# Optimization experiments

Measured on AMD Instinct MI355X. Metric: run time of the kernel, lower is better.

Reference implementation:

```python
import jax, jax.numpy as jnp
import numpy as np

B, S, H, NH = 1, 2048, 2048, 16
HD = H // NH
EPS = 1e-5
NEG = jnp.finfo(jnp.float32).min


def _alibi_slopes(n_heads):
    # standard Bloom alibi slopes (n_heads power of 2)
    start = 2.0 ** (-(2.0 ** -(np.log2(n_heads) - 3)))
    return start * (start ** np.arange(n_heads))


def setup_inputs() -> dict:
    key = jax.random.key(0)
    ks = jax.random.split(key, 10)
    s = 0.02
    hidden_states = jax.random.normal(ks[0], (B, S, H), jnp.float32)
    # causal mask: True = masked (future positions)
    causal = ~jnp.tril(jnp.ones((S, S), dtype=bool))
    attention_mask = causal[None, None, :, :]  # [1,1,S,S]
    # alibi bias [B*NH, 1, S]
    slopes = jnp.asarray(_alibi_slopes(NH), jnp.float32)  # [NH]
    pos = jnp.arange(S, dtype=jnp.float32)
    alibi = (slopes[:, None] * pos[None, :])[:, None, :]  # [NH,1,S]
    alibi = jnp.tile(alibi, (B, 1, 1))  # [B*NH,1,S]
    return {
        "hidden_states": hidden_states,
        "attention_mask": attention_mask,
        "alibi": alibi,
        "head_mask": 0,
        "ln1_g": jnp.ones((H,), jnp.float32),
        "ln1_b": jnp.zeros((H,), jnp.float32),
        "qkv_w": jax.random.normal(ks[1], (3 * H, H), jnp.float32) * s,
        "qkv_b": jnp.zeros((3 * H,), jnp.float32),
        "dense_w": jax.random.normal(ks[2], (H, H), jnp.float32) * s,
        "dense_b": jnp.zeros((H,), jnp.float32),
        "ln2_g": jnp.ones((H,), jnp.float32),
        "ln2_b": jnp.zeros((H,), jnp.float32),
        "fc1_w": jax.random.normal(ks[3], (4 * H, H), jnp.float32) * s,
        "fc1_b": jnp.zeros((4 * H,), jnp.float32),
        "fc2_w": jax.random.normal(ks[4], (H, 4 * H), jnp.float32) * s,
        "fc2_b": jnp.zeros((H,), jnp.float32),
    }


def _ln(x, g, b):
    mu = jnp.mean(x, axis=-1, keepdims=True)
    var = jnp.mean(jnp.square(x - mu), axis=-1, keepdims=True)
    return (x - mu) * jax.lax.rsqrt(var + EPS) * g + b


def _gelu(x):
    # Bloom tanh-approx GELU
    return x * 0.5 * (1.0 + jnp.tanh(0.79788456 * x * (1.0 + 0.044715 * x * x)))


def reference(hidden_states, attention_mask, alibi, head_mask,
              ln1_g, ln1_b, qkv_w, qkv_b, dense_w, dense_b,
              ln2_g, ln2_b, fc1_w, fc1_b, fc2_w, fc2_b):
    b, s, h = hidden_states.shape
    x = _ln(hidden_states, ln1_g, ln1_b)
    residual = hidden_states  # apply_residual_connection_post_layernorm=False

    qkv = x @ qkv_w.T + qkv_b                      # [b,s,3H]
    qkv = qkv.reshape(b, s, NH, 3, HD)             # per-head interleaved
    q, k, v = qkv[..., 0, :], qkv[..., 1, :], qkv[..., 2, :]  # [b,s,nh,hd]

    inv = 1.0 / jnp.sqrt(jnp.float32(HD))
    scores = jnp.einsum('bqnd,bknd->bnqk', q, k) * inv  # [b,nh,s,s]
    scores = scores + alibi.reshape(b, NH, 1, s)
    scores = jnp.where(attention_mask, NEG, scores)
    w = jax.nn.softmax(scores, axis=-1)
    # head_mask == 0 -> falsy in original; no head masking applied
    ctx = jnp.einsum('bnqk,bknd->bqnd', w, v).reshape(b, s, h)
    attn_out = ctx @ dense_w.T + dense_b + residual

    y = _ln(attn_out, ln2_g, ln2_b)
    residual2 = attn_out
    hdn = _gelu(y @ fc1_w.T + fc1_b)
    out = hdn @ fc2_w.T + fc2_b + residual2
    return out
```

## Files before the change

### kernel.cpp

```cpp
#include <hip/hip_runtime.h>
#include <hip/hip_bf16.h>

#define SQ 2048
#define HH 2048
#define NHEAD 16
#define HD 128
#define QKVW (NHEAD*3*HD)

typedef __attribute__((ext_vector_type(8))) short bf16x8;
typedef __attribute__((ext_vector_type(4))) float f32x4;
typedef __attribute__((ext_vector_type(16))) float f32x16;

__device__ inline unsigned short f2bf(float f) {
    union { float f; unsigned u; } x; x.f = f;
    unsigned r = x.u + 0x7FFFu + ((x.u >> 16) & 1u);
    return (unsigned short)(r >> 16);
}

__device__ inline unsigned pack_bf2(float a, float b) {
    return (unsigned)f2bf(a) | ((unsigned)f2bf(b) << 16);
}

__device__ inline float gelu_f(float x) {
    float x3 = x * (1.f + 0.044715f * x * x);
    return 0.5f * x * (1.f + tanhf(0.79788456f * x3));
}

__device__ inline void gld16(void* lds, const void* g) {
    __builtin_amdgcn_global_load_lds(
        (__attribute__((address_space(1))) void*)(g),
        (__attribute__((address_space(3))) void*)(lds), 16, 0, 0);
}

__global__ __launch_bounds__(256) void ln_kernel(
    const float* __restrict__ in, const float* __restrict__ g,
    const float* __restrict__ b, unsigned short* __restrict__ out)
{
    int row = blockIdx.x;
    int t = threadIdx.x, lane = t & 63, wid = t >> 6;
    const float4* rp = (const float4*)(in + (size_t)row * HH);
    float4 v0 = rp[t], v1 = rp[t + 256];
    float s  = v0.x + v0.y + v0.z + v0.w + v1.x + v1.y + v1.z + v1.w;
    float ss = v0.x*v0.x + v0.y*v0.y + v0.z*v0.z + v0.w*v0.w
             + v1.x*v1.x + v1.y*v1.y + v1.z*v1.z + v1.w*v1.w;
    #pragma unroll
    for (int o = 32; o; o >>= 1) { s += __shfl_down(s, o); ss += __shfl_down(ss, o); }
    __shared__ float r0[4], r1[4];
    if (lane == 0) { r0[wid] = s; r1[wid] = ss; }
    __syncthreads();
    s  = r0[0] + r0[1] + r0[2] + r0[3];
    ss = r1[0] + r1[1] + r1[2] + r1[3];
    float mu = s * (1.f / HH);
    float var = ss * (1.f / HH) - mu * mu;
    float rs = rsqrtf(var + 1e-5f);
    float4 g0 = ((const float4*)g)[t], g1 = ((const float4*)g)[t + 256];
    float4 b0 = ((const float4*)b)[t], b1 = ((const float4*)b)[t + 256];
    ushort4 o0, o1;
    o0.x = f2bf((v0.x - mu) * rs * g0.x + b0.x);
    o0.y = f2bf((v0.y - mu) * rs * g0.y + b0.y);
    o0.z = f2bf((v0.z - mu) * rs * g0.z + b0.z);
    o0.w = f2bf((v0.w - mu) * rs * g0.w + b0.w);
    o1.x = f2bf((v1.x - mu) * rs * g1.x + b1.x);
    o1.y = f2bf((v1.y - mu) * rs * g1.y + b1.y);
    o1.z = f2bf((v1.z - mu) * rs * g1.z + b1.z);
    o1.w = f2bf((v1.w - mu) * rs * g1.w + b1.w);
    ushort4* op = (ushort4*)(out + (size_t)row * HH);
    op[t] = o0; op[t + 256] = o1;
}

__global__ __launch_bounds__(256) void reduce4_kernel(
    const float* __restrict__ p0, const float* __restrict__ p1,
    const float* __restrict__ p2, const float* __restrict__ p3,
    const float* __restrict__ res, const float* __restrict__ bias,
    float* __restrict__ out, int n4, int nc4m1)
{
    int i = blockIdx.x * blockDim.x + threadIdx.x;
    int st = gridDim.x * blockDim.x;
    for (; i < n4; i += st) {
        float4 a = ((const float4*)p0)[i];
        float4 b = ((const float4*)p1)[i];
        float4 c = ((const float4*)p2)[i];
        float4 d = ((const float4*)p3)[i];
        float4 r = ((const float4*)res)[i];
        float4 bv = ((const float4*)bias)[i & nc4m1];
        float4 o;
        o.x = a.x + b.x + c.x + d.x + r.x + bv.x;
        o.y = a.y + b.y + c.y + d.y + r.y + bv.y;
        o.z = a.z + b.z + c.z + d.z + r.z + bv.z;
        o.w = a.w + b.w + c.w + d.w + r.w + bv.w;
        ((float4*)out)[i] = o;
    }
}


template<int MODE, int GELU_ON>
__global__ __launch_bounds__(512, 4) void gemm256(
    const unsigned short* __restrict__ A, const float* __restrict__ B,
    const float* __restrict__ bias, void* __restrict__ outp,
    unsigned short* __restrict__ vtb, void* __restrict__ outp_hi,
    int N, int lda, int ldb, int kLen, int CH, int CW)
{
    __shared__ __align__(16) unsigned short Asm[2][256][32];
    __shared__ __align__(16) unsigned short Bsm[2][128][40];

    int t = threadIdx.x, lane = t & 63, wid = t >> 6;
    int lo = lane & 15, hi = lane >> 4;
    int wr = wid >> 2, wc = wid & 3;

    int id = (blockIdx.z * gridDim.y + blockIdx.y) * gridDim.x + blockIdx.x;
    int xcd = id & 7, local = id >> 3;
    int cgx = gridDim.x / CW;
    int cr = xcd / cgx, cc = xcd - cr * cgx;
    int lr = local / CW, lc = local - lr * CW;
    int R  = cr * CH + lr;
    int bn = cc * CW + lc;
    int bm = R % gridDim.y;
    int bz = R / gridDim.y;
    int m0 = bm * 256, n0 = bn * 128;
    int kstart = bz * kLen;
    int nt = kLen >> 5;

    int rA0 = wid * 16 + (lane >> 2);
    int sAc = lane & 3;
    int rB = t >> 2, pB = t & 3;

    const unsigned short* Abase = A + (size_t)m0 * lda + kstart;
    int s0 = (rA0 & 3) ^ ((rA0 >> 2) & 3);
    const unsigned short* Asrc0 = Abase + (size_t)rA0 * lda + ((sAc ^ s0) << 3);
    const unsigned short* Asrc1 = Abase + (size_t)(rA0 + 128) * lda + ((sAc ^ s0) << 3);
    const float* Bsrc = B + (size_t)(n0 + rB) * ldb + kstart + pB * 8;

    {
        float4 b0 = *(const float4*)(Bsrc);
        float4 b1 = *(const float4*)(Bsrc + 4);
        gld16(&Asm[0][wid * 16][0], Asrc0);
        gld16(&Asm[0][128 + wid * 16][0], Asrc1);
        int4 w;
        w.x = (int)pack_bf2(b0.x, b0.y); w.y = (int)pack_bf2(b0.z, b0.w);
        w.z = (int)pack_bf2(b1.x, b1.y); w.w = (int)pack_bf2(b1.z, b1.w);
        *(int4*)&Bsm[0][rB][pB * 8] = w;
        __syncthreads();
    }

    f32x4 acc[8][2] = {};
    for (int u = 0; u < nt; u++) {
        int buf = u & 1, nbuf = buf ^ 1;
        int t1 = (u + 1 < nt) ? u + 1 : u;
        float4 b0 = *(const float4*)(Bsrc + t1 * 32);
        float4 b1 = *(const float4*)(Bsrc + t1 * 32 + 4);
        gld16(&Asm[nbuf][wid * 16][0], Asrc0 + t1 * 32);
        gld16(&Asm[nbuf][128 + wid * 16][0], Asrc1 + t1 * 32);
        __builtin_amdgcn_s_setprio(1);
        const unsigned short (*LA)[32] = Asm[buf];
        const unsigned short (*LB)[40] = Bsm[buf];
        bf16x8 bfr0 = *(const bf16x8*)&LB[wc * 32 + lo][hi * 8];
        bf16x8 bfr1 = *(const bf16x8*)&LB[wc * 32 + 16 + lo][hi * 8];
        #pragma unroll
        for (int i = 0; i < 8; i++) {
            int rA = wr * 128 + i * 16 + lo;
            bf16x8 af = *(const bf16x8*)&LA[rA][(hi ^ ((rA & 3) ^ ((rA >> 2) & 3))) << 3];
            acc[i][0] = __builtin_amdgcn_mfma_f32_16x16x32_bf16(bfr0, af, acc[i][0], 0, 0, 0);
            acc[i][1] = __builtin_amdgcn_mfma_f32_16x16x32_bf16(bfr1, af, acc[i][1], 0, 0, 0);
        }
        __builtin_amdgcn_s_setprio(0);
        int4 w;
        w.x = (int)pack_bf2(b0.x, b0.y); w.y = (int)pack_bf2(b0.z, b0.w);
        w.z = (int)pack_bf2(b1.x, b1.y); w.w = (int)pack_bf2(b1.z, b1.w);
        *(int4*)&Bsm[nbuf][rB][pB * 8] = w;
        __syncthreads();
    }

    if (MODE == 0) {
        float* po = ((bz < 2) ? (float*)outp : (float*)outp_hi)
                  + (size_t)(bz & 1) * SQ * (size_t)N;
        #pragma unroll
        for (int i = 0; i < 8; i++) {
            int gr = m0 + wr * 128 + i * 16 + lo;
            #pragma unroll
            for (int c = 0; c < 2; c++) {
                int gc = n0 + wc * 32 + c * 16 + hi * 4;
                *(f32x4*)&po[(size_t)gr * N + gc] = acc[i][c];
            }
        }
    } else if (MODE == 1) {
        unsigned short* op = (unsigned short*)outp;
        #pragma unroll
        for (int i = 0; i < 8; i++) {
            int gr = m0 + wr * 128 + i * 16 + lo;
            #pragma unroll
            for (int c = 0; c < 2; c++) {
                int gc = n0 + wc * 32 + c * 16 + hi * 4;
                float4 bi = *(const float4*)&bias[gc];
                float v0 = acc[i][c][0] + bi.x, v1 = acc[i][c][1] + bi.y;
                float v2 = acc[i][c][2] + bi.z, v3 = acc[i][c][3] + bi.w;
                if (GELU_ON) { v0 = gelu_f(v0); v1 = gelu_f(v1); v2 = gelu_f(v2); v3 = gelu_f(v3); }
                ushort4 o; o.x = f2bf(v0); o.y = f2bf(v1); o.z = f2bf(v2); o.w = f2bf(v3);
                *(ushort4*)&op[(size_t)gr * N + gc] = o;
            }
        }
    } else {
        unsigned short* op = (unsigned short*)outp;
        int head = n0 / 384;
        int cat = (n0 >> 7) % 3;
        #pragma unroll
        for (int i = 0; i < 8; i++) {
            int gr = m0 + wr * 128 + i * 16 + lo;
            #pragma unroll
            for (int c = 0; c < 2; c++) {
                int gc = n0 + wc * 32 + c * 16 + hi * 4;
                float4 bi = *(const float4*)&bias[gc];
                float v0 = acc[i][c][0] + bi.x, v1 = acc[i][c][1] + bi.y;
                float v2 = acc[i][c][2] + bi.z, v3 = acc[i][c][3] + bi.w;
                if (cat == 2) {
                    int d = wc * 32 + c * 16 + hi * 4;
                    unsigned short* vp = vtb + (size_t)(head * HD + d) * SQ + gr;
                    vp[0]      = f2bf(v0);
                    vp[SQ]     = f2bf(v1);
                    vp[2 * SQ] = f2bf(v2);
                    vp[3 * SQ] = f2bf(v3);
                } else {
                    ushort4 o; o.x = f2bf(v0); o.y = f2bf(v1); o.z = f2bf(v2); o.w = f2bf(v3);
                    *(ushort4*)&op[(size_t)gr * N + gc] = o;
                }
            }
        }
    }
}

__global__ __launch_bounds__(128) void attn_kernel(
    const unsigned short* __restrict__ qkvB,
    const unsigned short* __restrict__ vtb,
    unsigned short* __restrict__ ctx)
{
    int w = blockIdx.x;
    int lid = (w & 7) * 64 + (w >> 3);
    int n = lid >> 5, qt = lid & 31;
    int t = threadIdx.x, lane = t & 63, wid = t >> 6;
    int l32 = lane & 31, h2 = lane >> 5;
    int q0 = qt * 64, qg = q0 + wid * 32 + l32;

    __shared__ __align__(16) unsigned short Ks[64][128];
    __shared__ __align__(16) unsigned short Vt[128][64];

    bf16x8 qf[8];
    const unsigned short* qp = qkvB + (size_t)qg * QKVW + n * 384 + h2 * 8;
    #pragma unroll
    for (int d8 = 0; d8 < 8; d8++)
        qf[d8] = *(const bf16x8*)(qp + d8 * 16);

    const float slope = exp2f(-0.5f * (float)(n + 1));
    const float inv = 0.08838834764831845f;
    float m = -INFINITY, lsum = 0.f;
    f32x16 ao[4] = {};

    int krow = lane >> 4, kch = lane & 15;
    int vrow = lane >> 3, vch = lane & 7;
    const unsigned short* kb_ = qkvB + n * 384 + 128;
    const unsigned short* vb_ = vtb + (size_t)n * HD * SQ;
    const char* ksb = (const char*)&Ks[0][0];
    const char* vsb = (const char*)&Vt[0][0];

    int nkb = qt + 1;
    for (int kb = 0; kb < nkb; kb++) {
        int k0 = kb * 64;
        __syncthreads();
        #pragma unroll
        for (int s = 0; s < 8; s++) {
            int r = wid * 32 + s * 4 + krow;
            gld16(&Ks[wid * 32 + s * 4][0],
                  kb_ + (size_t)(k0 + r) * QKVW + ((kch ^ (r & 7)) << 3));
            int dd = wid * 64 + s * 8 + vrow;
            gld16(&Vt[wid * 64 + s * 8][0],
                  vb_ + (size_t)dd * SQ + k0 + ((vch ^ (dd & 7)) << 3));
        }
        __syncthreads();

        f32x16 sc0 = {}, sc1 = {};
        #pragma unroll
        for (int d8 = 0; d8 < 8; d8++) {
            int ch = ((d8 * 2 + h2) ^ (l32 & 7)) << 4;
            bf16x8 kf0 = *(const bf16x8*)(ksb + l32 * 256 + ch);
            bf16x8 kf1 = *(const bf16x8*)(ksb + (32 + l32) * 256 + ch);
            sc0 = __builtin_amdgcn_mfma_f32_32x32x16_bf16(kf0, qf[d8], sc0, 0, 0, 0);
            sc1 = __builtin_amdgcn_mfma_f32_32x32x16_bf16(kf1, qf[d8], sc1, 0, 0, 0);
        }

        float tmax = -INFINITY;
        int last = (kb == nkb - 1);
        #pragma unroll
        for (int r = 0; r < 16; r++) {
            int kl = (r & 3) + 8 * (r >> 2) + 4 * h2;
            float s0 = sc0[r] * inv + slope * (float)(k0 + kl);
            float s1 = sc1[r] * inv + slope * (float)(k0 + 32 + kl);
            if (last) {
                if (k0 + kl > qg) s0 = -INFINITY;
                if (k0 + 32 + kl > qg) s1 = -INFINITY;
            }
            sc0[r] = s0; sc1[r] = s1;
            tmax = fmaxf(tmax, fmaxf(s0, s1));
        }
        tmax = fmaxf(tmax, __shfl_xor(tmax, 32));
        if (!__all(tmax <= m + 8.f)) {
            float mnew = fmaxf(m, tmax);
            float sca = __expf(m - mnew);
            m = mnew;
            lsum *= sca;
            #pragma unroll
            for (int db = 0; db < 4; db++)
                #pragma unroll
                for (int e = 0; e < 16; e++) ao[db][e] *= sca;
        }
        float psum = 0.f;
        #pragma unroll
        for (int r = 0; r < 16; r++) {
            sc0[r] = __expf(sc0[r] - m); psum += sc0[r];
            sc1[r] = __expf(sc1[r] - m); psum += sc1[r];
        }
        psum += __shfl_xor(psum, 32);
        lsum += psum;

        #pragma unroll
        for (int kstep = 0; kstep < 4; kstep++) {
            const int ks1 = kstep & 1;
            float a0, a1, a2, a3, b0, b1, b2, b3;
            if (kstep < 2) {
                a0 = sc0[8*ks1+0]; a1 = sc0[8*ks1+1]; a2 = sc0[8*ks1+2]; a3 = sc0[8*ks1+3];
                b0 = sc0[8*ks1+4]; b1 = sc0[8*ks1+5]; b2 = sc0[8*ks1+6]; b3 = sc0[8*ks1+7];
            } else {
                a0 = sc1[8*ks1+0]; a1 = sc1[8*ks1+1]; a2 = sc1[8*ks1+2]; a3 = sc1[8*ks1+3];
                b0 = sc1[8*ks1+4]; b1 = sc1[8*ks1+5]; b2 = sc1[8*ks1+6]; b3 = sc1[8*ks1+7];
            }
            unsigned ku0 = pack_bf2(h2 ? b0 : a0, h2 ? b1 : a1);
            unsigned ku1 = pack_bf2(h2 ? b2 : a2, h2 ? b3 : a3);
            unsigned su0 = pack_bf2(h2 ? a0 : b0, h2 ? a1 : b1);
            unsigned su1 = pack_bf2(h2 ? a2 : b2, h2 ? a3 : b3);
            unsigned r0 = (unsigned)__shfl_xor((int)su0, 32);
            unsigned r1 = (unsigned)__shfl_xor((int)su1, 32);
            union { int4 i; bf16x8 v; } u;
            u.i.x = h2 ? (int)r0  : (int)ku0;
            u.i.y = h2 ? (int)r1  : (int)ku1;
            u.i.z = h2 ? (int)ku0 : (int)r0;
            u.i.w = h2 ? (int)ku1 : (int)r1;
            bf16x8 pf = u.v;
            int ch = ((kstep * 2 + h2) ^ (l32 & 7)) << 4;
            #pragma unroll
            for (int db = 0; db < 4; db++) {
                bf16x8 vf = *(const bf16x8*)(vsb + (db * 32 + l32) * 128 + ch);
                ao[db] = __builtin_amdgcn_mfma_f32_32x32x16_bf16(vf, pf, ao[db], 0, 0, 0);
            }
        }
    }

    float rl = 1.f / lsum;
    #pragma unroll
    for (int db = 0; db < 4; db++)
        #pragma unroll
        for (int g = 0; g < 4; g++) {
            ushort4 o;
            o.x = f2bf(ao[db][g*4+0] * rl);
            o.y = f2bf(ao[db][g*4+1] * rl);
            o.z = f2bf(ao[db][g*4+2] * rl);
            o.w = f2bf(ao[db][g*4+3] * rl);
            *(ushort4*)(ctx + (size_t)qg * HH + n * HD + db * 32 + g * 8 + h2 * 4) = o;
        }
}

extern "C" void kernel_launch(void* const* d_in, const int* in_sizes, int n_in,
                              void* d_out, int out_size, void* d_ws, size_t ws_size,
                              hipStream_t stream) {
    const float* hs    = (const float*)d_in[0];
    const float* ln1g  = (const float*)d_in[4];
    const float* ln1b  = (const float*)d_in[5];
    const float* qkvw  = (const float*)d_in[6];
    const float* qkvb  = (const float*)d_in[7];
    const float* dw    = (const float*)d_in[8];
    const float* db    = (const float*)d_in[9];
    const float* ln2g  = (const float*)d_in[10];
    const float* ln2b  = (const float*)d_in[11];
    const float* f1w   = (const float*)d_in[12];
    const float* f1b   = (const float*)d_in[13];
    const float* f2w   = (const float*)d_in[14];
    const float* f2b   = (const float*)d_in[15];
    float* out = (float*)d_out;

    char* ws = (char*)d_ws;
    size_t off = 0;
    auto alloc = [&](size_t nbytes) {
        void* p = ws + off; off += (nbytes + 255) & ~(size_t)255; return p;
    };
    unsigned short* xbf  = (unsigned short*)alloc((size_t)SQ * HH * 2);
    unsigned short* qkvB = (unsigned short*)alloc((size_t)SQ * QKVW * 2);
    unsigned short* vtB  = (unsigned short*)alloc((size_t)NHEAD * HD * SQ * 2);
    unsigned short* ctx  = (unsigned short*)alloc((size_t)SQ * HH * 2);
    float*          attn = (float*)alloc((size_t)SQ * HH * 4);
    unsigned short* y    = (unsigned short*)alloc((size_t)SQ * HH * 2);
    unsigned short* hdn  = (unsigned short*)alloc((size_t)SQ * 4 * HH * 2);
    float*          extra = (float*)alloc((size_t)2 * SQ * HH * 4);

    const size_t PQ = (size_t)SQ * HH;
    float* part = (float*)ws;

    ln_kernel<<<SQ, 256, 0, stream>>>(hs, ln1g, ln1b, xbf);

    gemm256<2, 0><<<dim3(QKVW / 128, SQ / 256, 1), 512, 0, stream>>>(
        xbf, qkvw, qkvb, qkvB, vtB, nullptr, QKVW, HH, HH, HH, 4, 12);

    attn_kernel<<<512, 128, 0, stream>>>(qkvB, vtB, ctx);

    gemm256<0, 0><<<dim3(HH / 128, SQ / 256, 4), 512, 0, stream>>>(
        ctx, dw, nullptr, part, nullptr, hdn, HH, HH, HH, HH / 4, 8, 8);
    reduce4_kernel<<<2048, 256, 0, stream>>>(
        part, part + PQ, (float*)hdn, (float*)hdn + PQ, hs, db, attn, SQ * HH / 4, HH / 4 - 1);

    ln_kernel<<<SQ, 256, 0, stream>>>(attn, ln2g, ln2b, y);

    gemm256<1, 1><<<dim3(4 * HH / 128, SQ / 256, 1), 512, 0, stream>>>(
        y, f1w, f1b, hdn, nullptr, nullptr, 4 * HH, HH, HH, HH, 4, 16);

    gemm256<0, 0><<<dim3(HH / 128, SQ / 256, 4), 512, 0, stream>>>(
        hdn, f2w, nullptr, part, nullptr, extra, HH, 4 * HH, 4 * HH, HH, 8, 8);
    reduce4_kernel<<<2048, 256, 0, stream>>>(
        part, part + PQ, extra, extra + PQ, attn, f2b, out, SQ * HH / 4, HH / 4 - 1);
}
```

Before: 484.0 us.

## Triple-buffer GEMM LDS stages with prefetch distance two and swizzled B tile

Changes the bf16 GEMM main loop from double to triple buffering. A tiles are loaded two steps ahead, and B fp32 values are held in registers one step before being packed into LDS. The full __syncthreads is replaced by explicit vmcnt/lgkmcnt waits plus s_barrier, so some global loads can stay in flight across iterations. The padded B LDS row is replaced with an XOR swizzle to avoid bank conflicts without padding. This uses more LDS, which may lower occupancy, and the hand-counted waitcnt values must exactly match the number of outstanding loads.

```diff
diff --git a/kernel.cpp b/kernel.cpp
--- a/kernel.cpp
+++ b/kernel.cpp
@@ -100,8 +100,8 @@
     unsigned short* __restrict__ vtb, void* __restrict__ outp_hi,
     int N, int lda, int ldb, int kLen, int CH, int CW)
 {
-    __shared__ __align__(16) unsigned short Asm[2][256][32];
-    __shared__ __align__(16) unsigned short Bsm[2][128][40];
+    __shared__ __align__(16) unsigned short Asm[3][256][32];
+    __shared__ __align__(16) unsigned short Bsm[3][128][32];
 
     int t = threadIdx.x, lane = t & 63, wid = t >> 6;
     int lo = lane & 15, hi = lane >> 4;
@@ -129,45 +129,61 @@
     const unsigned short* Asrc0 = Abase + (size_t)rA0 * lda + ((sAc ^ s0) << 3);
     const unsigned short* Asrc1 = Abase + (size_t)(rA0 + 128) * lda + ((sAc ^ s0) << 3);
     const float* Bsrc = B + (size_t)(n0 + rB) * ldb + kstart + pB * 8;
-
+    int wBc = (pB ^ (rB & 3)) << 3;
+
+    gld16(&Asm[0][wid * 16][0], Asrc0);
+    gld16(&Asm[0][128 + wid * 16][0], Asrc1);
+    float4 c0 = *(const float4*)(Bsrc);
+    float4 c1 = *(const float4*)(Bsrc + 4);
+    int k1 = (nt > 1) ? 32 : 0;
+    gld16(&Asm[1][wid * 16][0], Asrc0 + k1);
+    gld16(&Asm[1][128 + wid * 16][0], Asrc1 + k1);
+    float4 d0 = *(const float4*)(Bsrc + k1);
+    float4 d1 = *(const float4*)(Bsrc + k1 + 4);
     {
-        float4 b0 = *(const float4*)(Bsrc);
-        float4 b1 = *(const float4*)(Bsrc + 4);
-        gld16(&Asm[0][wid * 16][0], Asrc0);
-        gld16(&Asm[0][128 + wid * 16][0], Asrc1);
         int4 w;
-        w.x = (int)pack_bf2(b0.x, b0.y); w.y = (int)pack_bf2(b0.z, b0.w);
-        w.z = (int)pack_bf2(b1.x, b1.y); w.w = (int)pack_bf2(b1.z, b1.w);
-        *(int4*)&Bsm[0][rB][pB * 8] = w;
-        __syncthreads();
+        w.x = (int)pack_bf2(c0.x, c0.y); w.y = (int)pack_bf2(c0.z, c0.w);
+        w.z = (int)pack_bf2(c1.x, c1.y); w.w = (int)pack_bf2(c1.z, c1.w);
+        *(int4*)&Bsm[0][rB][wBc] = w;
     }
+    float4 bo0 = d0, bo1 = d1;
+    asm volatile("s_waitcnt vmcnt(2) lgkmcnt(0)" ::: "memory");
+    __builtin_amdgcn_s_barrier();
 
     f32x4 acc[8][2] = {};
+    int sl0 = 0, sl1 = 1, sl2 = 2;
     for (int u = 0; u < nt; u++) {
-        int buf = u & 1, nbuf = buf ^ 1;
-        int t1 = (u + 1 < nt) ? u + 1 : u;
-        float4 b0 = *(const float4*)(Bsrc + t1 * 32);
-        float4 b1 = *(const float4*)(Bsrc + t1 * 32 + 4);
-        gld16(&Asm[nbuf][wid * 16][0], Asrc0 + t1 * 32);
-        gld16(&Asm[nbuf][128 + wid * 16][0], Asrc1 + t1 * 32);
+        int t2 = (u + 2 < nt) ? u + 2 : nt - 1;
+        gld16(&Asm[sl2][wid * 16][0], Asrc0 + t2 * 32);
+        gld16(&Asm[sl2][128 + wid * 16][0], Asrc1 + t2 * 32);
+        float4 bn0 = *(const float4*)(Bsrc + t2 * 32);
+        float4 bn1 = *(const float4*)(Bsrc + t2 * 32 + 4);
+        {
+            int4 w;
+            w.x = (int)pack_bf2(bo0.x, bo0.y); w.y = (int)pack_bf2(bo0.z, bo0.w);
+            w.z = (int)pack_bf2(bo1.x, bo1.y); w.w = (int)pack_bf2(bo1.z, bo1.w);
+            *(int4*)&Bsm[sl1][rB][wBc] = w;
+        }
         __builtin_amdgcn_s_setprio(1);
-        const unsigned short (*LA)[32] = Asm[buf];
-        const unsigned short (*LB)[40] = Bsm[buf];
-        bf16x8 bfr0 = *(const bf16x8*)&LB[wc * 32 + lo][hi * 8];
-        bf16x8 bfr1 = *(const bf16x8*)&LB[wc * 32 + 16 + lo][hi * 8];
-        #pragma unroll
-        for (int i = 0; i < 8; i++) {
-            int rA = wr * 128 + i * 16 + lo;
-            bf16x8 af = *(const bf16x8*)&LA[rA][(hi ^ ((rA & 3) ^ ((rA >> 2) & 3))) << 3];
-            acc[i][0] = __builtin_amdgcn_mfma_f32_16x16x32_bf16(bfr0, af, acc[i][0], 0, 0, 0);
-            acc[i][1] = __builtin_amdgcn_mfma_f32_16x16x32_bf16(bfr1, af, acc[i][1], 0, 0, 0);
+        {
+            const unsigned short (*LA)[32] = Asm[sl0];
+            const unsigned short (*LB)[32] = Bsm[sl0];
+            int rB0 = wc * 32 + lo, rB1 = wc * 32 + 16 + lo;
+            bf16x8 bfr0 = *(const bf16x8*)&LB[rB0][(hi ^ (rB0 & 3)) << 3];
+            bf16x8 bfr1 = *(const bf16x8*)&LB[rB1][(hi ^ (rB1 & 3)) << 3];
+            #pragma unroll
+            for (int i = 0; i < 8; i++) {
+                int rA = wr * 128 + i * 16 + lo;
+                bf16x8 af = *(const bf16x8*)&LA[rA][(hi ^ ((rA & 3) ^ ((rA >> 2) & 3))) << 3];
+                acc[i][0] = __builtin_amdgcn_mfma_f32_16x16x32_bf16(bfr0, af, acc[i][0], 0, 0, 0);
+                acc[i][1] = __builtin_amdgcn_mfma_f32_16x16x32_bf16(bfr1, af, acc[i][1], 0, 0, 0);
+            }
         }
         __builtin_amdgcn_s_setprio(0);
-        int4 w;
-        w.x = (int)pack_bf2(b0.x, b0.y); w.y = (int)pack_bf2(b0.z, b0.w);
-        w.z = (int)pack_bf2(b1.x, b1.y); w.w = (int)pack_bf2(b1.z, b1.w);
-        *(int4*)&Bsm[nbuf][rB][pB * 8] = w;
-        __syncthreads();
+        bo0 = bn0; bo1 = bn1;
+        asm volatile("s_waitcnt vmcnt(4) lgkmcnt(0)" ::: "memory");
+        __builtin_amdgcn_s_barrier();
+        int tmp = sl0; sl0 = sl1; sl1 = sl2; sl2 = tmp;
     }
 
     if (MODE == 0) {
```

After: 480.6 us. About the same (-0.7%).

## Switch GEMMs to 128x128 tiles with 4 waves and deeper B prefetch

Applied to the files above, without the earlier changes.

Replaces the 256x128, 8-wave GEMM with a 128x128, 4-wave kernel. Each wave now computes a 64x64 sub-tile (4x4 MFMAs), which raises fragment reuse per LDS read. B loads are prefetched two iterations ahead in registers, converted, and stored to LDS before the compute step. The A swizzle is simplified and the grid and XCD-mapping parameters are adjusted. This doubles the number of blocks and B-tile reloads, and it raises register pressure per thread.

```diff
diff --git a/kernel.cpp b/kernel.cpp
--- a/kernel.cpp
+++ b/kernel.cpp
@@ -94,18 +94,18 @@
 
 
 template<int MODE, int GELU_ON>
-__global__ __launch_bounds__(512, 4) void gemm256(
+__global__ __launch_bounds__(256, 4) void gemm128(
     const unsigned short* __restrict__ A, const float* __restrict__ B,
     const float* __restrict__ bias, void* __restrict__ outp,
     unsigned short* __restrict__ vtb, void* __restrict__ outp_hi,
     int N, int lda, int ldb, int kLen, int CH, int CW)
 {
-    __shared__ __align__(16) unsigned short Asm[2][256][32];
+    __shared__ __align__(16) unsigned short Asm[2][128][32];
     __shared__ __align__(16) unsigned short Bsm[2][128][40];
 
     int t = threadIdx.x, lane = t & 63, wid = t >> 6;
     int lo = lane & 15, hi = lane >> 4;
-    int wr = wid >> 2, wc = wid & 3;
+    int wr = wid >> 1, wc = wid & 1;
 
     int id = (blockIdx.z * gridDim.y + blockIdx.y) * gridDim.x + blockIdx.x;
     int xcd = id & 7, local = id >> 3;
@@ -116,57 +116,80 @@
     int bn = cc * CW + lc;
     int bm = R % gridDim.y;
     int bz = R / gridDim.y;
-    int m0 = bm * 256, n0 = bn * 128;
+    int m0 = bm * 128, n0 = bn * 128;
     int kstart = bz * kLen;
     int nt = kLen >> 5;
 
-    int rA0 = wid * 16 + (lane >> 2);
-    int sAc = lane & 3;
-    int rB = t >> 2, pB = t & 3;
-
+    int rA = wid * 16 + (lane >> 2);
     const unsigned short* Abase = A + (size_t)m0 * lda + kstart;
-    int s0 = (rA0 & 3) ^ ((rA0 >> 2) & 3);
-    const unsigned short* Asrc0 = Abase + (size_t)rA0 * lda + ((sAc ^ s0) << 3);
-    const unsigned short* Asrc1 = Abase + (size_t)(rA0 + 128) * lda + ((sAc ^ s0) << 3);
-    const float* Bsrc = B + (size_t)(n0 + rB) * ldb + kstart + pB * 8;
-
+    const unsigned short* Asrc0 = Abase + (size_t)rA * lda + (((lane & 3) ^ (rA & 3)) << 3);
+    const unsigned short* Asrc1 = Asrc0 + (size_t)64 * lda;
+    int rB = t & 127, hseg = t >> 7;
+    const float* Bsrc = B + (size_t)(n0 + rB) * ldb + kstart + hseg * 16;
+
+    gld16(&Asm[0][wid * 16][0], Asrc0);
+    gld16(&Asm[0][64 + wid * 16][0], Asrc1);
+    float4 q0 = *(const float4*)(Bsrc);
+    float4 q1 = *(const float4*)(Bsrc + 4);
+    float4 q2 = *(const float4*)(Bsrc + 8);
+    float4 q3 = *(const float4*)(Bsrc + 12);
     {
-        float4 b0 = *(const float4*)(Bsrc);
-        float4 b1 = *(const float4*)(Bsrc + 4);
-        gld16(&Asm[0][wid * 16][0], Asrc0);
-        gld16(&Asm[0][128 + wid * 16][0], Asrc1);
-        int4 w;
-        w.x = (int)pack_bf2(b0.x, b0.y); w.y = (int)pack_bf2(b0.z, b0.w);
-        w.z = (int)pack_bf2(b1.x, b1.y); w.w = (int)pack_bf2(b1.z, b1.w);
-        *(int4*)&Bsm[0][rB][pB * 8] = w;
-        __syncthreads();
+        int4 w0, w1;
+        w0.x = (int)pack_bf2(q0.x, q0.y); w0.y = (int)pack_bf2(q0.z, q0.w);
+        w0.z = (int)pack_bf2(q1.x, q1.y); w0.w = (int)pack_bf2(q1.z, q1.w);
+        w1.x = (int)pack_bf2(q2.x, q2.y); w1.y = (int)pack_bf2(q2.z, q2.w);
+        w1.z = (int)pack_bf2(q3.x, q3.y); w1.w = (int)pack_bf2(q3.z, q3.w);
+        *(int4*)&Bsm[0][rB][hseg * 16] = w0;
+        *(int4*)&Bsm[0][rB][hseg * 16 + 8] = w1;
     }
-
-    f32x4 acc[8][2] = {};
+    int k1 = (nt > 1) ? 32 : 0;
+    float4 p0 = *(const float4*)(Bsrc + k1);
+    float4 p1 = *(const float4*)(Bsrc + k1 + 4);
+    float4 p2 = *(const float4*)(Bsrc + k1 + 8);
+    float4 p3 = *(const float4*)(Bsrc + k1 + 12);
+    __syncthreads();
+
+    f32x4 acc[4][4] = {};
     for (int u = 0; u < nt; u++) {
         int buf = u & 1, nbuf = buf ^ 1;
-        int t1 = (u + 1 < nt) ? u + 1 : u;
-        float4 b0 = *(const float4*)(Bsrc + t1 * 32);
-        float4 b1 = *(const float4*)(Bsrc + t1 * 32 + 4);
+        int t1 = (u + 1 < nt) ? u + 1 : nt - 1;
+        int t2 = (u + 2 < nt) ? u + 2 : nt - 1;
+        {
+            int4 w0, w1;
+            w0.x = (int)pack_bf2(p0.x, p0.y); w0.y = (int)pack_bf2(p0.z, p0.w);
+            w0.z = (int)pack_bf2(p1.x, p1.y); w0.w = (int)pack_bf2(p1.z, p1.w);
+            w1.x = (int)pack_bf2(p2.x, p2.y); w1.y = (int)pack_bf2(p2.z, p2.w);
+            w1.z = (int)pack_bf2(p3.x, p3.y); w1.w = (int)pack_bf2(p3.z, p3.w);
+            *(int4*)&Bsm[nbuf][rB][hseg * 16] = w0;
+            *(int4*)&Bsm[nbuf][rB][hseg * 16 + 8] = w1;
+        }
         gld16(&Asm[nbuf][wid * 16][0], Asrc0 + t1 * 32);
-        gld16(&Asm[nbuf][128 + wid * 16][0], Asrc1 + t1 * 32);
+        gld16(&Asm[nbuf][64 + wid * 16][0], Asrc1 + t1 * 32);
+        p0 = *(const float4*)(Bsrc + t2 * 32);
+        p1 = *(const float4*)(Bsrc + t2 * 32 + 4);
+        p2 = *(const float4*)(Bsrc + t2 * 32 + 8);
+        p3 = *(const float4*)(Bsrc + t2 * 32 + 12);
         __builtin_amdgcn_s_setprio(1);
-        const unsigned short (*LA)[32] = Asm[buf];
-        const unsigned short (*LB)[40] = Bsm[buf];
-        bf16x8 bfr0 = *(const bf16x8*)&LB[wc * 32 + lo][hi * 8];
-        bf16x8 bfr1 = *(const bf16x8*)&LB[wc * 32 + 16 + lo][hi * 8];
-        #pragma unroll
-        for (int i = 0; i < 8; i++) {
-            int rA = wr * 128 + i * 16 + lo;
-            bf16x8 af = *(const bf16x8*)&LA[rA][(hi ^ ((rA & 3) ^ ((rA >> 2) & 3))) << 3];
-            acc[i][0] = __builtin_amdgcn_mfma_f32_16x16x32_bf16(bfr0, af, acc[i][0], 0, 0, 0);
-            acc[i][1] = __builtin_amdgcn_mfma_f32_16x16x32_bf16(bfr1, af, acc[i][1], 0, 0, 0);
+        {
+            const unsigned short (*LA)[32] = Asm[buf];
+            const unsigned short (*LB)[40] = Bsm[buf];
+            bf16x8 af[4], bfr[4];
+            #pragma unroll
+            for (int i = 0; i < 4; i++) {
+                int r = wr * 64 + i * 16 + lo;
+                af[i] = *(const bf16x8*)&LA[r][(hi ^ (lo & 3)) << 3];
+            }
+            #pragma unroll
+            for (int c = 0; c < 4; c++)
+                bfr[c] = *(const bf16x8*)&LB[wc * 64 + c * 16 + lo][hi * 8];
+            #pragma unroll
+            for (int i = 0; i < 4; i++)
+                #pragma unroll
+                for (int c = 0; c < 4; c++)
+                    acc[i][c] = __builtin_amdgcn_mfma_f32_16x16x32_bf16(
+                        bfr[c], af[i], acc[i][c], 0, 0, 0);
         }
         __builtin_amdgcn_s_setprio(0);
-        int4 w;
-        w.x = (int)pack_bf2(b0.x, b0.y); w.y = (int)pack_bf2(b0.z, b0.w);
-        w.z = (int)pack_bf2(b1.x, b1.y); w.w = (int)pack_bf2(b1.z, b1.w);
-        *(int4*)&Bsm[nbuf][rB][pB * 8] = w;
         __syncthreads();
     }
 
@@ -174,22 +197,22 @@
         float* po = ((bz < 2) ? (float*)outp : (float*)outp_hi)
                   + (size_t)(bz & 1) * SQ * (size_t)N;
         #pragma unroll
-        for (int i = 0; i < 8; i++) {
-            int gr = m0 + wr * 128 + i * 16 + lo;
-            #pragma unroll
-            for (int c = 0; c < 2; c++) {
-                int gc = n0 + wc * 32 + c * 16 + hi * 4;
+        for (int i = 0; i < 4; i++) {
+            int gr = m0 + wr * 64 + i * 16 + lo;
+            #pragma unroll
+            for (int c = 0; c < 4; c++) {
+                int gc = n0 + wc * 64 + c * 16 + hi * 4;
                 *(f32x4*)&po[(size_t)gr * N + gc] = acc[i][c];
             }
         }
     } else if (MODE == 1) {
         unsigned short* op = (unsigned short*)outp;
         #pragma unroll
-        for (int i = 0; i < 8; i++) {
-            int gr = m0 + wr * 128 + i * 16 + lo;
-            #pragma unroll
-            for (int c = 0; c < 2; c++) {
-                int gc = n0 + wc * 32 + c * 16 + hi * 4;
+        for (int i = 0; i < 4; i++) {
+            int gr = m0 + wr * 64 + i * 16 + lo;
+            #pragma unroll
+            for (int c = 0; c < 4; c++) {
+                int gc = n0 + wc * 64 + c * 16 + hi * 4;
                 float4 bi = *(const float4*)&bias[gc];
                 float v0 = acc[i][c][0] + bi.x, v1 = acc[i][c][1] + bi.y;
                 float v2 = acc[i][c][2] + bi.z, v3 = acc[i][c][3] + bi.w;
@@ -203,16 +226,16 @@
         int head = n0 / 384;
         int cat = (n0 >> 7) % 3;
         #pragma unroll
-        for (int i = 0; i < 8; i++) {
-            int gr = m0 + wr * 128 + i * 16 + lo;
-            #pragma unroll
-            for (int c = 0; c < 2; c++) {
-                int gc = n0 + wc * 32 + c * 16 + hi * 4;
+        for (int i = 0; i < 4; i++) {
+            int gr = m0 + wr * 64 + i * 16 + lo;
+            #pragma unroll
+            for (int c = 0; c < 4; c++) {
+                int gc = n0 + wc * 64 + c * 16 + hi * 4;
                 float4 bi = *(const float4*)&bias[gc];
                 float v0 = acc[i][c][0] + bi.x, v1 = acc[i][c][1] + bi.y;
                 float v2 = acc[i][c][2] + bi.z, v3 = acc[i][c][3] + bi.w;
                 if (cat == 2) {
-                    int d = wc * 32 + c * 16 + hi * 4;
+                    int d = wc * 64 + c * 16 + hi * 4;
                     unsigned short* vp = vtb + (size_t)(head * HD + d) * SQ + gr;
                     vp[0]      = f2bf(v0);
                     vp[SQ]     = f2bf(v1);
@@ -402,23 +425,23 @@
 
     ln_kernel<<<SQ, 256, 0, stream>>>(hs, ln1g, ln1b, xbf);
 
-    gemm256<2, 0><<<dim3(QKVW / 128, SQ / 256, 1), 512, 0, stream>>>(
-        xbf, qkvw, qkvb, qkvB, vtB, nullptr, QKVW, HH, HH, HH, 4, 12);
+    gemm128<2, 0><<<dim3(QKVW / 128, SQ / 128, 1), 256, 0, stream>>>(
+        xbf, qkvw, qkvb, qkvB, vtB, nullptr, QKVW, HH, HH, HH, 8, 12);
 
     attn_kernel<<<512, 128, 0, stream>>>(qkvB, vtB, ctx);
 
-    gemm256<0, 0><<<dim3(HH / 128, SQ / 256, 4), 512, 0, stream>>>(
-        ctx, dw, nullptr, part, nullptr, hdn, HH, HH, HH, HH / 4, 8, 8);
+    gemm128<0, 0><<<dim3(HH / 128, SQ / 128, 4), 256, 0, stream>>>(
+        ctx, dw, nullptr, part, nullptr, hdn, HH, HH, HH, HH / 4, 8, 16);
     reduce4_kernel<<<2048, 256, 0, stream>>>(
         part, part + PQ, (float*)hdn, (float*)hdn + PQ, hs, db, attn, SQ * HH / 4, HH / 4 - 1);
 
     ln_kernel<<<SQ, 256, 0, stream>>>(attn, ln2g, ln2b, y);
 
-    gemm256<1, 1><<<dim3(4 * HH / 128, SQ / 256, 1), 512, 0, stream>>>(
-        y, f1w, f1b, hdn, nullptr, nullptr, 4 * HH, HH, HH, HH, 4, 16);
-
-    gemm256<0, 0><<<dim3(HH / 128, SQ / 256, 4), 512, 0, stream>>>(
-        hdn, f2w, nullptr, part, nullptr, extra, HH, 4 * HH, 4 * HH, HH, 8, 8);
+    gemm128<1, 1><<<dim3(4 * HH / 128, SQ / 128, 1), 256, 0, stream>>>(
+        y, f1w, f1b, hdn, nullptr, nullptr, 4 * HH, HH, HH, HH, 8, 16);
+
+    gemm128<0, 0><<<dim3(HH / 128, SQ / 128, 4), 256, 0, stream>>>(
+        hdn, f2w, nullptr, part, nullptr, extra, HH, 4 * HH, 4 * HH, HH, 8, 16);
     reduce4_kernel<<<2048, 256, 0, stream>>>(
         part, part + PQ, extra, extra + PQ, attn, f2b, out, SQ * HH / 4, HH / 4 - 1);
 }
```

New measurement: 718.2 us. 1.48x slower.

## Switch GEMM to 32x32x16 MFMA tiles and prefetch B two stages ahead

Applied to the files above, without the earlier changes.

Replaces the 16x16x32 bf16 MFMA inner loop with 32x32x16 MFMAs, so each wave issues fewer, larger matrix instructions and does fewer LDS fragment reads per output. The A-tile LDS swizzle and row assignment change to match the new fragment layout, and the epilogues are remapped to the 32x32 accumulator layout. B fp32 loads are now issued two iterations ahead in registers and their bf16 conversion and LDS store happen before compute, which deepens the pipeline at the cost of extra live registers under the 512-thread, 4-block launch bound.

```diff
diff --git a/kernel.cpp b/kernel.cpp
--- a/kernel.cpp
+++ b/kernel.cpp
@@ -104,7 +104,7 @@
     __shared__ __align__(16) unsigned short Bsm[2][128][40];
 
     int t = threadIdx.x, lane = t & 63, wid = t >> 6;
-    int lo = lane & 15, hi = lane >> 4;
+    int l32 = lane & 31, h2 = lane >> 5;
     int wr = wid >> 2, wc = wid & 3;
 
     int id = (blockIdx.z * gridDim.y + blockIdx.y) * gridDim.x + blockIdx.x;
@@ -120,53 +120,59 @@
     int kstart = bz * kLen;
     int nt = kLen >> 5;
 
-    int rA0 = wid * 16 + (lane >> 2);
-    int sAc = lane & 3;
-    int rB = t >> 2, pB = t & 3;
-
+    int r0_ = wid * 32 + (lane >> 2);
+    int r1_ = r0_ + 16;
     const unsigned short* Abase = A + (size_t)m0 * lda + kstart;
-    int s0 = (rA0 & 3) ^ ((rA0 >> 2) & 3);
-    const unsigned short* Asrc0 = Abase + (size_t)rA0 * lda + ((sAc ^ s0) << 3);
-    const unsigned short* Asrc1 = Abase + (size_t)(rA0 + 128) * lda + ((sAc ^ s0) << 3);
-    const float* Bsrc = B + (size_t)(n0 + rB) * ldb + kstart + pB * 8;
-
+    const unsigned short* Asrc0 = Abase + (size_t)r0_ * lda
+                                + (((lane & 3) ^ ((r0_ >> 1) & 3)) << 3);
+    const unsigned short* Asrc1 = Abase + (size_t)r1_ * lda
+                                + (((lane & 3) ^ ((r1_ >> 1) & 3)) << 3);
+    int rB = t >> 2, cB = t & 3;
+    const float* Bsrc = B + (size_t)(n0 + rB) * ldb + kstart + cB * 8;
+
+    gld16(&Asm[0][wid * 32][0], Asrc0);
+    gld16(&Asm[0][wid * 32 + 16][0], Asrc1);
     {
-        float4 b0 = *(const float4*)(Bsrc);
-        float4 b1 = *(const float4*)(Bsrc + 4);
-        gld16(&Asm[0][wid * 16][0], Asrc0);
-        gld16(&Asm[0][128 + wid * 16][0], Asrc1);
+        float4 q0 = *(const float4*)(Bsrc);
+        float4 q1 = *(const float4*)(Bsrc + 4);
         int4 w;
-        w.x = (int)pack_bf2(b0.x, b0.y); w.y = (int)pack_bf2(b0.z, b0.w);
-        w.z = (int)pack_bf2(b1.x, b1.y); w.w = (int)pack_bf2(b1.z, b1.w);
-        *(int4*)&Bsm[0][rB][pB * 8] = w;
-        __syncthreads();
+        w.x = (int)pack_bf2(q0.x, q0.y); w.y = (int)pack_bf2(q0.z, q0.w);
+        w.z = (int)pack_bf2(q1.x, q1.y); w.w = (int)pack_bf2(q1.z, q1.w);
+        *(int4*)&Bsm[0][rB][cB * 8] = w;
     }
-
-    f32x4 acc[8][2] = {};
+    int k1 = (nt > 1) ? 32 : 0;
+    float4 p0_ = *(const float4*)(Bsrc + k1);
+    float4 p1_ = *(const float4*)(Bsrc + k1 + 4);
+    __syncthreads();
+
+    f32x16 acc[4] = {};
     for (int u = 0; u < nt; u++) {
         int buf = u & 1, nbuf = buf ^ 1;
-        int t1 = (u + 1 < nt) ? u + 1 : u;
-        float4 b0 = *(const float4*)(Bsrc + t1 * 32);
-        float4 b1 = *(const float4*)(Bsrc + t1 * 32 + 4);
-        gld16(&Asm[nbuf][wid * 16][0], Asrc0 + t1 * 32);
-        gld16(&Asm[nbuf][128 + wid * 16][0], Asrc1 + t1 * 32);
+        int t1 = ((u + 1 < nt) ? u + 1 : nt - 1) * 32;
+        int t2 = ((u + 2 < nt) ? u + 2 : nt - 1) * 32;
+        {
+            int4 w;
+            w.x = (int)pack_bf2(p0_.x, p0_.y); w.y = (int)pack_bf2(p0_.z, p0_.w);
+            w.z = (int)pack_bf2(p1_.x, p1_.y); w.w = (int)pack_bf2(p1_.z, p1_.w);
+            *(int4*)&Bsm[nbuf][rB][cB * 8] = w;
+        }
+        gld16(&Asm[nbuf][wid * 32][0], Asrc0 + t1);
+        gld16(&Asm[nbuf][wid * 32 + 16][0], Asrc1 + t1);
+        p0_ = *(const float4*)(Bsrc + t2);
+        p1_ = *(const float4*)(Bsrc + t2 + 4);
         __builtin_amdgcn_s_setprio(1);
-        const unsigned short (*LA)[32] = Asm[buf];
-        const unsigned short (*LB)[40] = Bsm[buf];
-        bf16x8 bfr0 = *(const bf16x8*)&LB[wc * 32 + lo][hi * 8];
-        bf16x8 bfr1 = *(const bf16x8*)&LB[wc * 32 + 16 + lo][hi * 8];
-        #pragma unroll
-        for (int i = 0; i < 8; i++) {
-            int rA = wr * 128 + i * 16 + lo;
-            bf16x8 af = *(const bf16x8*)&LA[rA][(hi ^ ((rA & 3) ^ ((rA >> 2) & 3))) << 3];
-            acc[i][0] = __builtin_amdgcn_mfma_f32_16x16x32_bf16(bfr0, af, acc[i][0], 0, 0, 0);
-            acc[i][1] = __builtin_amdgcn_mfma_f32_16x16x32_bf16(bfr1, af, acc[i][1], 0, 0, 0);
+        #pragma unroll
+        for (int ks = 0; ks < 2; ks++) {
+            bf16x8 bfr = *(const bf16x8*)&Bsm[buf][wc * 32 + l32][ks * 16 + h2 * 8];
+            #pragma unroll
+            for (int fi = 0; fi < 4; fi++) {
+                int r = wr * 128 + fi * 32 + l32;
+                bf16x8 af = *(const bf16x8*)
+                    &Asm[buf][r][(((ks * 2 + h2) ^ ((r >> 1) & 3))) << 3];
+                acc[fi] = __builtin_amdgcn_mfma_f32_32x32x16_bf16(bfr, af, acc[fi], 0, 0, 0);
+            }
         }
         __builtin_amdgcn_s_setprio(0);
-        int4 w;
-        w.x = (int)pack_bf2(b0.x, b0.y); w.y = (int)pack_bf2(b0.z, b0.w);
-        w.z = (int)pack_bf2(b1.x, b1.y); w.w = (int)pack_bf2(b1.z, b1.w);
-        *(int4*)&Bsm[nbuf][rB][pB * 8] = w;
         __syncthreads();
     }
 
@@ -174,25 +180,28 @@
         float* po = ((bz < 2) ? (float*)outp : (float*)outp_hi)
                   + (size_t)(bz & 1) * SQ * (size_t)N;
         #pragma unroll
-        for (int i = 0; i < 8; i++) {
-            int gr = m0 + wr * 128 + i * 16 + lo;
-            #pragma unroll
-            for (int c = 0; c < 2; c++) {
-                int gc = n0 + wc * 32 + c * 16 + hi * 4;
-                *(f32x4*)&po[(size_t)gr * N + gc] = acc[i][c];
+        for (int fi = 0; fi < 4; fi++) {
+            int gr = m0 + wr * 128 + fi * 32 + l32;
+            #pragma unroll
+            for (int g = 0; g < 4; g++) {
+                int gc = n0 + wc * 32 + g * 8 + h2 * 4;
+                float4 v;
+                v.x = acc[fi][g*4+0]; v.y = acc[fi][g*4+1];
+                v.z = acc[fi][g*4+2]; v.w = acc[fi][g*4+3];
+                *(float4*)&po[(size_t)gr * N + gc] = v;
             }
         }
     } else if (MODE == 1) {
         unsigned short* op = (unsigned short*)outp;
         #pragma unroll
-        for (int i = 0; i < 8; i++) {
-            int gr = m0 + wr * 128 + i * 16 + lo;
-            #pragma unroll
-            for (int c = 0; c < 2; c++) {
-                int gc = n0 + wc * 32 + c * 16 + hi * 4;
+        for (int fi = 0; fi < 4; fi++) {
+            int gr = m0 + wr * 128 + fi * 32 + l32;
+            #pragma unroll
+            for (int g = 0; g < 4; g++) {
+                int gc = n0 + wc * 32 + g * 8 + h2 * 4;
                 float4 bi = *(const float4*)&bias[gc];
-                float v0 = acc[i][c][0] + bi.x, v1 = acc[i][c][1] + bi.y;
-                float v2 = acc[i][c][2] + bi.z, v3 = acc[i][c][3] + bi.w;
+                float v0 = acc[fi][g*4+0] + bi.x, v1 = acc[fi][g*4+1] + bi.y;
+                float v2 = acc[fi][g*4+2] + bi.z, v3 = acc[fi][g*4+3] + bi.w;
                 if (GELU_ON) { v0 = gelu_f(v0); v1 = gelu_f(v1); v2 = gelu_f(v2); v3 = gelu_f(v3); }
                 ushort4 o; o.x = f2bf(v0); o.y = f2bf(v1); o.z = f2bf(v2); o.w = f2bf(v3);
                 *(ushort4*)&op[(size_t)gr * N + gc] = o;
@@ -203,16 +212,16 @@
         int head = n0 / 384;
         int cat = (n0 >> 7) % 3;
         #pragma unroll
-        for (int i = 0; i < 8; i++) {
-            int gr = m0 + wr * 128 + i * 16 + lo;
-            #pragma unroll
-            for (int c = 0; c < 2; c++) {
-                int gc = n0 + wc * 32 + c * 16 + hi * 4;
+        for (int fi = 0; fi < 4; fi++) {
+            int gr = m0 + wr * 128 + fi * 32 + l32;
+            #pragma unroll
+            for (int g = 0; g < 4; g++) {
+                int gc = n0 + wc * 32 + g * 8 + h2 * 4;
                 float4 bi = *(const float4*)&bias[gc];
-                float v0 = acc[i][c][0] + bi.x, v1 = acc[i][c][1] + bi.y;
-                float v2 = acc[i][c][2] + bi.z, v3 = acc[i][c][3] + bi.w;
+                float v0 = acc[fi][g*4+0] + bi.x, v1 = acc[fi][g*4+1] + bi.y;
+                float v2 = acc[fi][g*4+2] + bi.z, v3 = acc[fi][g*4+3] + bi.w;
                 if (cat == 2) {
-                    int d = wc * 32 + c * 16 + hi * 4;
+                    int d = wc * 32 + g * 8 + h2 * 4;
                     unsigned short* vp = vtb + (size_t)(head * HD + d) * SQ + gr;
                     vp[0]      = f2bf(v0);
                     vp[SQ]     = f2bf(v1);
```

After: 469.2 us. 1.03x faster.
